# Performance work log

Measured on AMD Instinct MI355X. Metric: run time of the kernel, lower is better.

Reference implementation:

```python
import jax, jax.numpy as jnp
import numpy as np


def setup_inputs() -> dict:
    key = jax.random.key(0)
    kq, kk, kv = jax.random.split(key, 3)
    n, d = 8192, 128
    Q = jax.random.normal(kq, (n, d), dtype=jnp.float32)
    K = jax.random.normal(kk, (n, d), dtype=jnp.float32)
    V = jax.random.normal(kv, (n, d), dtype=jnp.float32)
    return {"Q": Q, "K": K, "V": V}


def reference(Q, K, V):
    # The blockwise online-softmax loops in the torch module compute exactly
    # softmax(Q @ K^T) @ V  -- note: NO 1/sqrt(d) scaling in the original.
    S = jnp.einsum('qd,kd->qk', Q, K)          # [n, n] scores
    P = jax.nn.softmax(S, axis=-1)             # numerically stable softmax
    O = jnp.einsum('qk,kd->qd', P, V)          # [n, d]
    return O
```

## Files before the change

### kernel.cpp

```cpp
#include <hip/hip_runtime.h>
#include <hip/hip_bf16.h>

#define N 8192
#define D 128
#define NSPLIT 8
#define KVSPLIT (N / NSPLIT)
#define KVBLK 64
#define NT (KVSPLIT / KVBLK)

typedef __attribute__((ext_vector_type(8))) _Float16 half8;
typedef __attribute__((ext_vector_type(2))) __fp16 fp16x2;
typedef __attribute__((ext_vector_type(16))) float f32x16;

union H8 { fp16x2 h2[4]; half8 h8; };

__global__ void cvt_f16_4(const float4* __restrict__ src, _Float16* __restrict__ dst, int n4) {
    int i = blockIdx.x * 256 + threadIdx.x;
    if (i < n4) {
        float4 v = src[i];
        _Float16 o0 = (_Float16)v.x, o1 = (_Float16)v.y, o2 = (_Float16)v.z, o3 = (_Float16)v.w;
        ushort4 o;
        o.x = __builtin_bit_cast(ushort, o0);
        o.y = __builtin_bit_cast(ushort, o1);
        o.z = __builtin_bit_cast(ushort, o2);
        o.w = __builtin_bit_cast(ushort, o3);
        *reinterpret_cast<ushort4*>(dst + i * 4) = o;
    }
}

__global__ void transpose_v(const float* __restrict__ V, _Float16* __restrict__ Vtp) {
    __shared__ _Float16 tile[64][65];
    const int k0 = blockIdx.x * 64;
    const int d0 = blockIdx.y * 64;
    const int tid = threadIdx.x;
#pragma unroll
    for (int p = 0; p < 16; ++p) {
        int flat = p * 256 + tid;
        int r = flat >> 6, cc = flat & 63;
        tile[r][cc] = (_Float16)(V[(size_t)(k0 + r) * D + d0 + cc]);
    }
    __syncthreads();
#pragma unroll
    for (int p = 0; p < 16; ++p) {
        int flat = p * 256 + tid;
        int dd = flat >> 6, kl = flat & 63;
        int kk = kl & 31;
        int s32 = 16 * (kk >> 4) + 8 * ((kk >> 2) & 1) + 4 * ((kk >> 3) & 1) + (kk & 3);
        Vtp[(size_t)(d0 + dd) * N + k0 + (kl & 32) + s32] = tile[kl][dd];
    }
}

#define STAGE(kdst_, vdst_, kbase_)                                                   \
    {                                                                                 \
        _Pragma("unroll")                                                             \
        for (int p = 0; p < 4; ++p) {                                                 \
            int c4 = p * 256 + tid;                                                   \
            int row = c4 >> 4, chs = c4 & 15;                                         \
            int cc = (chs & 8) | ((chs & 7) ^ (row & 7));                             \
            __builtin_amdgcn_global_load_lds(                                         \
                (const __attribute__((address_space(1))) void*)(Kh + (size_t)((kbase_) + row) * D + cc * 8), \
                (__attribute__((address_space(3))) void*)((kdst_) + c4 * 8), 16, 0, 0);              \
        }                                                                             \
        _Pragma("unroll")                                                             \
        for (int p = 0; p < 4; ++p) {                                                 \
            int c4 = p * 256 + tid;                                                   \
            int dd = c4 >> 3, chs = c4 & 7;                                           \
            int cc = chs ^ (dd & 7);                                                  \
            __builtin_amdgcn_global_load_lds(                                         \
                (const __attribute__((address_space(1))) void*)(Vtp + (size_t)dd * N + (kbase_) + cc * 8),   \
                (__attribute__((address_space(3))) void*)((vdst_) + c4 * 8), 16, 0, 0);              \
        }                                                                             \
    }

#define PVSTEP(Pv, ktc)                                                               \
    _Pragma("unroll")                                                                 \
    for (int ks = 0; ks < 2; ++ks) {                                                  \
        H8 u;                                                                         \
        u.h2[0] = __builtin_amdgcn_cvt_pkrtz(Pv[ks * 8 + 0], Pv[ks * 8 + 1]);         \
        u.h2[1] = __builtin_amdgcn_cvt_pkrtz(Pv[ks * 8 + 2], Pv[ks * 8 + 3]);         \
        u.h2[2] = __builtin_amdgcn_cvt_pkrtz(Pv[ks * 8 + 4], Pv[ks * 8 + 5]);         \
        u.h2[3] = __builtin_amdgcn_cvt_pkrtz(Pv[ks * 8 + 6], Pv[ks * 8 + 7]);         \
        int ch = (ktc) * 4 + ks * 2 + h;                                              \
        _Pragma("unroll")                                                             \
        for (int dt = 0; dt < 4; ++dt) {                                              \
            int dd = dt * 32 + c;                                                     \
            int pos = ch ^ (dd & 7);                                                  \
            half8 vf = *reinterpret_cast<const half8*>(vb + dd * 64 + pos * 8);       \
            oacc[dt] = __builtin_amdgcn_mfma_f32_32x32x16_f16(vf, u.h8, oacc[dt], 0, 0, 0); \
        }                                                                             \
    }

__launch_bounds__(256, 2)
__global__ void fa_kernel(const _Float16* __restrict__ Qh, const _Float16* __restrict__ Kh,
                          const _Float16* __restrict__ Vtp, _Float16* __restrict__ Oph,
                          float* __restrict__ Mpart, float* __restrict__ Lpart) {
    __shared__ __align__(16) _Float16 smem[32768];

    const int tid  = threadIdx.x;
    const int w    = tid >> 6;
    const int lane = tid & 63;
    const int h    = lane >> 5;
    const int c    = lane & 31;
    const int bid  = blockIdx.x;
    const int split = bid & 7;
    const int bx   = bid >> 3;
    const int q0w  = bx * 128 + w * 32;
    const int kv0  = split * KVSPLIT;

    half8 qa[8];
    {
        const _Float16* qrow = Qh + (size_t)(q0w + c) * D + h * 8;
#pragma unroll
        for (int st = 0; st < 8; ++st)
            qa[st] = *reinterpret_cast<const half8*>(qrow + st * 16);
    }

    f32x16 oacc[4];
#pragma unroll
    for (int dt = 0; dt < 4; ++dt)
#pragma unroll
        for (int r = 0; r < 16; ++r) oacc[dt][r] = 0.f;
    float mrun = -1e30f, lrun = 0.f;

    STAGE(smem, smem + 16384, kv0);
    __syncthreads();

    for (int t = 0; t < NT; ++t) {
        const int cur = t & 1;
        if (t + 1 < NT)
            STAGE(smem + (cur ^ 1) * 8192, smem + 16384 + (cur ^ 1) * 8192, kv0 + (t + 1) * KVBLK);

        const _Float16* kb = smem + cur * 8192;
        const _Float16* vb = smem + 16384 + cur * 8192;

        f32x16 sb0, sb1;
#pragma unroll
        for (int r = 0; r < 16; ++r) { sb0[r] = 0.f; sb1[r] = 0.f; }
#pragma unroll
        for (int st = 0; st < 8; ++st) {
            int ch = st * 2 + h;
            int pos = (ch & 8) | ((ch & 7) ^ (c & 7));
            half8 kf0 = *reinterpret_cast<const half8*>(kb + c * 128 + pos * 8);
            half8 kf1 = *reinterpret_cast<const half8*>(kb + (32 + c) * 128 + pos * 8);
            sb0 = __builtin_amdgcn_mfma_f32_32x32x16_f16(kf0, qa[st], sb0, 0, 0, 0);
            sb1 = __builtin_amdgcn_mfma_f32_32x32x16_f16(kf1, qa[st], sb1, 0, 0, 0);
        }

        float pmax = sb0[0];
#pragma unroll
        for (int r = 1; r < 16; ++r) pmax = fmaxf(pmax, sb0[r]);
#pragma unroll
        for (int r = 0; r < 16; ++r) pmax = fmaxf(pmax, sb1[r]);
        pmax = fmaxf(pmax, __shfl_xor(pmax, 32));

        if (!__all(pmax <= mrun + 8.0f)) {
            float nm = fmaxf(mrun, pmax);
            float scl = __expf(mrun - nm);
            lrun *= scl;
#pragma unroll
            for (int dt = 0; dt < 4; ++dt)
#pragma unroll
                for (int r = 0; r < 16; ++r) oacc[dt][r] *= scl;
            mrun = nm;
        }
        float tsum = 0.f;
#pragma unroll
        for (int r = 0; r < 16; ++r) { sb0[r] = __expf(sb0[r] - mrun); tsum += sb0[r]; }
#pragma unroll
        for (int r = 0; r < 16; ++r) { sb1[r] = __expf(sb1[r] - mrun); tsum += sb1[r]; }
        lrun += tsum + __shfl_xor(tsum, 32);

        PVSTEP(sb0, 0)
        PVSTEP(sb1, 1)

        __syncthreads();
    }

    __syncthreads();
    float inv = 1.0f / lrun;
    float* epi = reinterpret_cast<float*>(smem) + w * 1088;
    const size_t sbase = (size_t)split * N;
#pragma unroll
    for (int dt = 0; dt < 4; ++dt) {
#pragma unroll
        for (int r = 0; r < 16; ++r) {
            int dloc = (r & 3) + 8 * (r >> 2) + 4 * h;
            epi[c * 33 + dloc] = oacc[dt][r] * inv;
        }
#pragma unroll
        for (int it = 0; it < 16; ++it) {
            int j = it * 64 + lane;
            int rr = j >> 5, cc2 = j & 31;
            Oph[(sbase + q0w + rr) * D + dt * 32 + cc2] = (_Float16)epi[rr * 33 + cc2];
        }
    }
    if (h == 0) {
        Mpart[sbase + q0w + c] = mrun;
        Lpart[sbase + q0w + c] = lrun;
    }
}

__global__ void fa_merge(const _Float16* __restrict__ Oph, const float* __restrict__ Mpart,
                         const float* __restrict__ Lpart, float* __restrict__ O) {
    int idx = blockIdx.x * 256 + threadIdx.x;
    int q = idx >> 7;
    int d = idx & 127;
    float m[NSPLIT];
    float M = -1e30f;
#pragma unroll
    for (int s = 0; s < NSPLIT; ++s) {
        m[s] = Mpart[s * N + q];
        M = fmaxf(M, m[s]);
    }
    float acc = 0.f, wsum = 0.f;
#pragma unroll
    for (int s = 0; s < NSPLIT; ++s) {
        float wgt = __expf(m[s] - M) * Lpart[s * N + q];
        acc += wgt * (float)Oph[((size_t)s * N + q) * D + d];
        wsum += wgt;
    }
    O[idx] = acc / wsum;
}

extern "C" void kernel_launch(void* const* d_in, const int* in_sizes, int n_in,
                              void* d_out, int out_size, void* d_ws, size_t ws_size,
                              hipStream_t stream) {
    const float* Q = (const float*)d_in[0];
    const float* K = (const float*)d_in[1];
    const float* V = (const float*)d_in[2];
    float* O = (float*)d_out;

    _Float16* Qh = (_Float16*)d_ws;
    _Float16* Kh = Qh + (size_t)N * D;
    _Float16* Vtp = Kh + (size_t)N * D;
    _Float16* Oph = Vtp + (size_t)N * D;
    float* Mpart = (float*)(Oph + (size_t)NSPLIT * N * D);
    float* Lpart = Mpart + (size_t)NSPLIT * N;

    const int n4 = N * D / 4;
    hipLaunchKernelGGL(cvt_f16_4, dim3(n4 / 256), dim3(256), 0, stream,
                       (const float4*)Q, Qh, n4);
    hipLaunchKernelGGL(cvt_f16_4, dim3(n4 / 256), dim3(256), 0, stream,
                       (const float4*)K, Kh, n4);
    hipLaunchKernelGGL(transpose_v, dim3(N / 64, D / 64), dim3(256), 0, stream, V, Vtp);
    hipLaunchKernelGGL(fa_kernel, dim3(64 * NSPLIT), dim3(256), 0, stream,
                       Qh, Kh, Vtp, Oph, Mpart, Lpart);
    hipLaunchKernelGGL(fa_merge, dim3(N * D / 256), dim3(256), 0, stream,
                       Oph, Mpart, Lpart, O);
}
```

Baseline: 64.32 us.

## Use 8-wave blocks, 16 KV splits, fused Q conversion and MFMA priority hints

Doubles the KV split count to 16 and moves the attention kernel to 512-thread blocks covering 256 query rows each. K/V staging is spread across the larger block. The separate Q fp32-to-fp16 conversion kernel is removed; Q is now converted in registers inside the attention kernel, and the first K/V stage is issued before that Q load so the two overlap. s_setprio hints raise wave priority around the MFMA sections. In exchange, the tighter launch bounds may force register spills, the merge must combine twice as many partials, and the partial-output workspace doubles.

```diff
diff --git a/kernel.cpp b/kernel.cpp
--- a/kernel.cpp
+++ b/kernel.cpp
@@ -3,10 +3,11 @@
 
 #define N 8192
 #define D 128
-#define NSPLIT 8
+#define NSPLIT 16
 #define KVSPLIT (N / NSPLIT)
 #define KVBLK 64
 #define NT (KVSPLIT / KVBLK)
+#define NWAVES 8
 
 typedef __attribute__((ext_vector_type(8))) _Float16 half8;
 typedef __attribute__((ext_vector_type(2))) __fp16 fp16x2;
@@ -53,8 +54,8 @@
 #define STAGE(kdst_, vdst_, kbase_)                                                   \
     {                                                                                 \
         _Pragma("unroll")                                                             \
-        for (int p = 0; p < 4; ++p) {                                                 \
-            int c4 = p * 256 + tid;                                                   \
+        for (int p = 0; p < 2; ++p) {                                                 \
+            int c4 = p * 512 + tid;                                                   \
             int row = c4 >> 4, chs = c4 & 15;                                         \
             int cc = (chs & 8) | ((chs & 7) ^ (row & 7));                             \
             __builtin_amdgcn_global_load_lds(                                         \
@@ -62,8 +63,8 @@
                 (__attribute__((address_space(3))) void*)((kdst_) + c4 * 8), 16, 0, 0);              \
         }                                                                             \
         _Pragma("unroll")                                                             \
-        for (int p = 0; p < 4; ++p) {                                                 \
-            int c4 = p * 256 + tid;                                                   \
+        for (int p = 0; p < 2; ++p) {                                                 \
+            int c4 = p * 512 + tid;                                                   \
             int dd = c4 >> 3, chs = c4 & 7;                                           \
             int cc = chs ^ (dd & 7);                                                  \
             __builtin_amdgcn_global_load_lds(                                         \
@@ -90,8 +91,8 @@
         }                                                                             \
     }
 
-__launch_bounds__(256, 2)
-__global__ void fa_kernel(const _Float16* __restrict__ Qh, const _Float16* __restrict__ Kh,
+__launch_bounds__(512, 4)
+__global__ void fa_kernel(const float* __restrict__ Qf, const _Float16* __restrict__ Kh,
                           const _Float16* __restrict__ Vtp, _Float16* __restrict__ Oph,
                           float* __restrict__ Mpart, float* __restrict__ Lpart) {
     __shared__ __align__(16) _Float16 smem[32768];
@@ -102,17 +103,25 @@
     const int h    = lane >> 5;
     const int c    = lane & 31;
     const int bid  = blockIdx.x;
-    const int split = bid & 7;
-    const int bx   = bid >> 3;
-    const int q0w  = bx * 128 + w * 32;
+    const int split = bid & (NSPLIT - 1);
+    const int bx   = bid >> 4;
+    const int q0w  = bx * 256 + w * 32;
     const int kv0  = split * KVSPLIT;
+
+    STAGE(smem, smem + 16384, kv0);
 
     half8 qa[8];
     {
-        const _Float16* qrow = Qh + (size_t)(q0w + c) * D + h * 8;
-#pragma unroll
-        for (int st = 0; st < 8; ++st)
-            qa[st] = *reinterpret_cast<const half8*>(qrow + st * 16);
+        const float* qrow = Qf + (size_t)(q0w + c) * D + h * 8;
+#pragma unroll
+        for (int st = 0; st < 8; ++st) {
+            float4 a = *reinterpret_cast<const float4*>(qrow + st * 16);
+            float4 b = *reinterpret_cast<const float4*>(qrow + st * 16 + 4);
+            half8 q;
+            q[0] = (_Float16)a.x; q[1] = (_Float16)a.y; q[2] = (_Float16)a.z; q[3] = (_Float16)a.w;
+            q[4] = (_Float16)b.x; q[5] = (_Float16)b.y; q[6] = (_Float16)b.z; q[7] = (_Float16)b.w;
+            qa[st] = q;
+        }
     }
 
     f32x16 oacc[4];
@@ -122,7 +131,6 @@
         for (int r = 0; r < 16; ++r) oacc[dt][r] = 0.f;
     float mrun = -1e30f, lrun = 0.f;
 
-    STAGE(smem, smem + 16384, kv0);
     __syncthreads();
 
     for (int t = 0; t < NT; ++t) {
@@ -136,6 +144,7 @@
         f32x16 sb0, sb1;
 #pragma unroll
         for (int r = 0; r < 16; ++r) { sb0[r] = 0.f; sb1[r] = 0.f; }
+        __builtin_amdgcn_s_setprio(1);
 #pragma unroll
         for (int st = 0; st < 8; ++st) {
             int ch = st * 2 + h;
@@ -145,6 +154,7 @@
             sb0 = __builtin_amdgcn_mfma_f32_32x32x16_f16(kf0, qa[st], sb0, 0, 0, 0);
             sb1 = __builtin_amdgcn_mfma_f32_32x32x16_f16(kf1, qa[st], sb1, 0, 0, 0);
         }
+        __builtin_amdgcn_s_setprio(0);
 
         float pmax = sb0[0];
 #pragma unroll
@@ -170,8 +180,10 @@
         for (int r = 0; r < 16; ++r) { sb1[r] = __expf(sb1[r] - mrun); tsum += sb1[r]; }
         lrun += tsum + __shfl_xor(tsum, 32);
 
+        __builtin_amdgcn_s_setprio(1);
         PVSTEP(sb0, 0)
         PVSTEP(sb1, 1)
+        __builtin_amdgcn_s_setprio(0);
 
         __syncthreads();
     }
@@ -230,8 +242,7 @@
     const float* V = (const float*)d_in[2];
     float* O = (float*)d_out;
 
-    _Float16* Qh = (_Float16*)d_ws;
-    _Float16* Kh = Qh + (size_t)N * D;
+    _Float16* Kh = (_Float16*)d_ws;
     _Float16* Vtp = Kh + (size_t)N * D;
     _Float16* Oph = Vtp + (size_t)N * D;
     float* Mpart = (float*)(Oph + (size_t)NSPLIT * N * D);
@@ -239,12 +250,10 @@
 
     const int n4 = N * D / 4;
     hipLaunchKernelGGL(cvt_f16_4, dim3(n4 / 256), dim3(256), 0, stream,
-                       (const float4*)Q, Qh, n4);
-    hipLaunchKernelGGL(cvt_f16_4, dim3(n4 / 256), dim3(256), 0, stream,
                        (const float4*)K, Kh, n4);
     hipLaunchKernelGGL(transpose_v, dim3(N / 64, D / 64), dim3(256), 0, stream, V, Vtp);
-    hipLaunchKernelGGL(fa_kernel, dim3(64 * NSPLIT), dim3(256), 0, stream,
-                       Qh, Kh, Vtp, Oph, Mpart, Lpart);
+    hipLaunchKernelGGL(fa_kernel, dim3((N / 256) * NSPLIT), dim3(512), 0, stream,
+                       Q, Kh, Vtp, Oph, Mpart, Lpart);
     hipLaunchKernelGGL(fa_merge, dim3(N * D / 256), dim3(256), 0, stream,
                        Oph, Mpart, Lpart, O);
 }
```

Result: slower. 235.5 us (+266.1%).
